# Kernel tuning notes

Measured on AMD Instinct MI355X. Metric: run time of the kernel, lower is better.

Reference implementation:

```python
import jax, jax.numpy as jnp
from jax import lax
import numpy as np

EPS_REG = 1.0     # ot.sinkhorn(..., M, 1, ...) hardcodes reg=1 in the original forward
N_ITER = 100      # max_iter: fixed stabilized (log-domain) Sinkhorn iterations


def setup_inputs() -> dict:
    key = jax.random.key(0)
    kx, ky = jax.random.split(key)
    x = jax.random.normal(kx, (1, 4096, 512), dtype=jnp.float32)
    y = jax.random.normal(ky, (1, 4096, 512), dtype=jnp.float32)
    return {"x": x, "y": y}


def _cost_matrix(x, y):
    x2 = jnp.sum(x * x, axis=-1)                      # [B, P1]
    y2 = jnp.sum(y * y, axis=-1)                      # [B, P2]
    xy = jnp.einsum("bpd,bqd->bpq", x, y)            # [B, P1, P2]
    return jnp.maximum(x2[:, :, None] + y2[:, None, :] - 2.0 * xy, 0.0)


def _sinkhorn_log(C, eps, n_iter):
    # Log-domain (stabilized) Sinkhorn with uniform marginals a=1/P1, b=1/P2.
    P1, P2 = C.shape
    eps_loga = eps * (-jnp.log(jnp.float32(P1)))
    eps_logb = eps * (-jnp.log(jnp.float32(P2)))

    def step(carry, _):
        f, g = carry
        f = eps_loga - eps * jax.nn.logsumexp((g[None, :] - C) / eps, axis=1)
        g = eps_logb - eps * jax.nn.logsumexp((f[:, None] - C) / eps, axis=0)
        return (f, g), None

    f0 = jnp.zeros((P1,), C.dtype)
    g0 = jnp.zeros((P2,), C.dtype)
    (f, g), _ = lax.scan(step, (f0, g0), None, length=n_iter)
    return jnp.exp((f[:, None] + g[None, :] - C) / eps)  # transport plan pi, rows sum to 1/P1


def reference(x, y):
    C = _cost_matrix(x, y)                                  # [B, P1, P2]
    pi = jax.vmap(lambda c: _sinkhorn_log(c, EPS_REG, N_ITER))(C)
    cost = jnp.sum(pi * C, axis=(-2, -1))                   # [B], reduction='none'
    return cost, pi, C
```

## Files before the change

kernel.cpp:

```cpp
#include <hip/hip_runtime.h>
#include <hip/hip_bf16.h>
#include <cstddef>

#define NROW 4096
#define DIM  512
static const size_t NP = (size_t)NROW * NROW;
#define ALPHA (-8.31776616671934f)

__global__ __launch_bounds__(256) void sqnorm_kernel(const float* __restrict__ x,
                                                     const float* __restrict__ y,
                                                     float* __restrict__ x2,
                                                     float* __restrict__ y2) {
    int gtid = blockIdx.x * 256 + threadIdx.x;
    int wid  = gtid >> 6;
    int lane = gtid & 63;
    const float* src = (wid < NROW) ? x : y;
    float*       dst = (wid < NROW) ? x2 : y2;
    int row = (wid < NROW) ? wid : (wid - NROW);
    const float4* r4 = (const float4*)(src + (size_t)row * DIM);
    float4 a = r4[lane];
    float4 b = r4[lane + 64];
    float s = a.x*a.x + a.y*a.y + a.z*a.z + a.w*a.w
            + b.x*b.x + b.y*b.y + b.z*b.z + b.w*b.w;
    #pragma unroll
    for (int off = 32; off > 0; off >>= 1) s += __shfl_down(s, off);
    if (lane == 0) dst[row] = s;
}

__global__ __launch_bounds__(256) void gemm_kernel(const float* __restrict__ A,
                                                   const float* __restrict__ B,
                                                   float* __restrict__ S) {
    __shared__ float As[16][132];
    __shared__ float Bs[16][132];
    const int bm = blockIdx.y * 128, bn = blockIdx.x * 128;
    const int tid = threadIdx.x;
    const int tx = tid & 15, ty = tid >> 4;
    float acc[8][8];
    #pragma unroll
    for (int i = 0; i < 8; ++i)
        #pragma unroll
        for (int j = 0; j < 8; ++j) acc[i][j] = 0.f;

    for (int kt = 0; kt < DIM; kt += 16) {
        #pragma unroll
        for (int h = 0; h < 2; ++h) {
            int f = tid + h * 256;
            int row = f >> 2, kk = (f & 3) << 2;
            float4 a4 = *(const float4*)(A + (size_t)(bm + row) * DIM + kt + kk);
            As[kk+0][row] = a4.x; As[kk+1][row] = a4.y;
            As[kk+2][row] = a4.z; As[kk+3][row] = a4.w;
            float4 b4 = *(const float4*)(B + (size_t)(bn + row) * DIM + kt + kk);
            Bs[kk+0][row] = b4.x; Bs[kk+1][row] = b4.y;
            Bs[kk+2][row] = b4.z; Bs[kk+3][row] = b4.w;
        }
        __syncthreads();
        #pragma unroll
        for (int k = 0; k < 16; ++k) {
            float ar[8], br[8];
            #pragma unroll
            for (int i = 0; i < 8; ++i) ar[i] = As[k][ty*8 + i];
            #pragma unroll
            for (int j = 0; j < 8; ++j) br[j] = Bs[k][tx*8 + j];
            #pragma unroll
            for (int i = 0; i < 8; ++i)
                #pragma unroll
                for (int j = 0; j < 8; ++j)
                    acc[i][j] = __fmaf_rn(ar[i], br[j], acc[i][j]);
        }
        __syncthreads();
    }
    #pragma unroll
    for (int i = 0; i < 8; ++i) {
        size_t off = (size_t)(bm + ty*8 + i) * NROW + bn + tx*8;
        #pragma unroll
        for (int j = 0; j < 8; ++j) S[off + j] = 2.0f * acc[i][j];
    }
}

__global__ __launch_bounds__(256) void transpose_kernel(const float* __restrict__ in,
                                                        float* __restrict__ out) {
    __shared__ float tile[64][65];
    int bx = blockIdx.x * 64, by = blockIdx.y * 64;
    int tx = threadIdx.x & 63, tw = threadIdx.x >> 6;
    #pragma unroll
    for (int r = tw; r < 64; r += 4)
        tile[r][tx] = in[(size_t)(by + r) * NROW + bx + tx];
    __syncthreads();
    #pragma unroll
    for (int r = tw; r < 64; r += 4)
        out[(size_t)(bx + r) * NROW + by + tx] = tile[tx][r];
}

__global__ void init_kernel(const float* __restrict__ y2,
                            float* __restrict__ gt,
                            float* __restrict__ cost) {
    int i = blockIdx.x * 256 + threadIdx.x;
    if (i < NROW) gt[i] = -y2[i];
    if (i == 0) cost[0] = 0.f;
}

__global__ __launch_bounds__(256) void lse_pass_kernel(const float* __restrict__ M,
                                                       const float* __restrict__ u,
                                                       float* __restrict__ outv) {
    const int row = blockIdx.x;
    const float* mrow = M + (size_t)row * NROW;
    const int t = threadIdx.x;
    float m = -3.0e38f, s = 0.f;
    #pragma unroll
    for (int h = 0; h < 16; ++h) {
        int j = t + h * 256;
        float v = u[j] + mrow[j];
        float d = v - m;
        float e = __expf(-fabsf(d));
        s = (d > 0.f) ? __fmaf_rn(s, e, 1.0f) : (s + e);
        m = fmaxf(m, v);
    }
    #pragma unroll
    for (int off = 1; off < 64; off <<= 1) {
        float m2 = __shfl_xor(m, off);
        float s2 = __shfl_xor(s, off);
        float d = m - m2;
        float e = __expf(-fabsf(d));
        s = (d > 0.f) ? __fmaf_rn(s2, e, s) : __fmaf_rn(s, e, s2);
        m = fmaxf(m, m2);
    }
    __shared__ float sm[4], ss[4];
    int lane = t & 63, w = t >> 6;
    if (lane == 0) { sm[w] = m; ss[w] = s; }
    __syncthreads();
    if (t == 0) {
        float M0 = sm[0], S0 = ss[0];
        #pragma unroll
        for (int w2 = 1; w2 < 4; ++w2) {
            float m2 = sm[w2], s2 = ss[w2];
            float d = M0 - m2;
            float e = __expf(-fabsf(d));
            S0 = (d > 0.f) ? __fmaf_rn(s2, e, S0) : __fmaf_rn(S0, e, s2);
            M0 = fmaxf(M0, m2);
        }
        outv[row] = ALPHA - (M0 + __logf(S0));
    }
}

__global__ __launch_bounds__(256) void finalize_kernel(const float* __restrict__ S,
                                                       const float* __restrict__ ft,
                                                       const float* __restrict__ gt,
                                                       const float* __restrict__ x2,
                                                       const float* __restrict__ y2,
                                                       float* __restrict__ pi,
                                                       float* __restrict__ C,
                                                       float* __restrict__ cost) {
    const int row = blockIdx.x;
    const size_t base = (size_t)row * NROW;
    const float fi  = ft[row];
    const float x2i = x2[row];
    float acc = 0.f;
    #pragma unroll
    for (int h = 0; h < 16; ++h) {
        int j = threadIdx.x + h * 256;
        float sv = S[base + j];
        float p  = __expf(fi + gt[j] + sv);
        float c  = fmaxf(x2i + y2[j] - sv, 0.f);
        pi[base + j] = p;
        C[base + j]  = c;
        acc = __fmaf_rn(p, c, acc);
    }
    #pragma unroll
    for (int off = 32; off > 0; off >>= 1) acc += __shfl_down(acc, off);
    __shared__ float sa[4];
    int lane = threadIdx.x & 63, w = threadIdx.x >> 6;
    if (lane == 0) sa[w] = acc;
    __syncthreads();
    if (threadIdx.x == 0)
        atomicAdd(cost, sa[0] + sa[1] + sa[2] + sa[3]);
}

extern "C" void kernel_launch(void* const* d_in, const int* in_sizes, int n_in,
                              void* d_out, int out_size, void* d_ws, size_t ws_size,
                              hipStream_t stream) {
    const float* x = (const float*)d_in[0];
    const float* y = (const float*)d_in[1];
    float* out  = (float*)d_out;
    float* cost = out;
    float* pi   = out + 1;
    float* Cpt  = out + 1 + NP;
    float* S  = Cpt;
    float* ST = pi;

    float* ws = (float*)d_ws;
    float* x2 = ws;
    float* y2 = ws + NROW;
    float* ft = ws + 2 * NROW;
    float* gt = ws + 3 * NROW;

    sqnorm_kernel<<<2048, 256, 0, stream>>>(x, y, x2, y2);
    gemm_kernel<<<dim3(32, 32), 256, 0, stream>>>(x, y, S);
    transpose_kernel<<<dim3(64, 64), 256, 0, stream>>>(S, ST);
    init_kernel<<<16, 256, 0, stream>>>(y2, gt, cost);

    for (int it = 0; it < 100; ++it) {
        lse_pass_kernel<<<NROW, 256, 0, stream>>>(S,  gt, ft);
        lse_pass_kernel<<<NROW, 256, 0, stream>>>(ST, ft, gt);
    }

    finalize_kernel<<<NROW, 256, 0, stream>>>(S, ft, gt, x2, y2, pi, Cpt, cost);
}
```

Measured before the change: 2.751 ms.

## Quantize cross-product matrix to int16 for Sinkhorn passes and use base-2 LSE

```diff
diff --git a/kernel.cpp b/kernel.cpp
--- a/kernel.cpp
+++ b/kernel.cpp
@@ -5,7 +5,12 @@
 #define NROW 4096
 #define DIM  512
 static const size_t NP = (size_t)NROW * NROW;
-#define ALPHA (-8.31776616671934f)
+#define L2E   1.4426950408889634f
+#define ALPHA2 (-12.0f)
+#define QSCALE 64.0f
+#define QD    (1.4426950408889634f / 64.0f)
+
+typedef unsigned int uint32;
 
 __global__ __launch_bounds__(256) void sqnorm_kernel(const float* __restrict__ x,
                                                      const float* __restrict__ y,
@@ -77,74 +82,120 @@
     }
 }
 
-__global__ __launch_bounds__(256) void transpose_kernel(const float* __restrict__ in,
-                                                        float* __restrict__ out) {
-    __shared__ float tile[64][65];
-    int bx = blockIdx.x * 64, by = blockIdx.y * 64;
-    int tx = threadIdx.x & 63, tw = threadIdx.x >> 6;
-    #pragma unroll
-    for (int r = tw; r < 64; r += 4)
-        tile[r][tx] = in[(size_t)(by + r) * NROW + bx + tx];
+__global__ __launch_bounds__(256) void quantA_kernel(const float* __restrict__ S,
+                                                     uint32* __restrict__ Sq) {
+    size_t i = (size_t)blockIdx.x * 256 + threadIdx.x;
+    const size_t nu = NP / 2, stride = (size_t)2048 * 256;
+    for (; i < nu; i += stride) {
+        float a = S[2*i], b = S[2*i + 1];
+        float qa = fmaxf(fminf(a * QSCALE,  32767.f), -32767.f);
+        float qb = fmaxf(fminf(b * QSCALE,  32767.f), -32767.f);
+        int ia = __float2int_rn(qa), ib = __float2int_rn(qb);
+        Sq[i] = (uint32)(ia & 0xffff) | ((uint32)ib << 16);
+    }
+}
+
+__global__ __launch_bounds__(256) void quantT_kernel(const float* __restrict__ S,
+                                                     uint32* __restrict__ SqT) {
+    __shared__ short tile[64][66];
+    const int bx = blockIdx.x * 64, by = blockIdx.y * 64;
+    const int t = threadIdx.x;
+    const int c = t & 63, r0 = t >> 6;
+    #pragma unroll
+    for (int rr = 0; rr < 16; ++rr) {
+        int r = r0 + rr * 4;
+        float v = S[(size_t)(by + r) * NROW + bx + c];
+        float q = fmaxf(fminf(v * QSCALE, 32767.f), -32767.f);
+        tile[r][c] = (short)__float2int_rn(q);
+    }
     __syncthreads();
-    #pragma unroll
-    for (int r = tw; r < 64; r += 4)
-        out[(size_t)(bx + r) * NROW + by + tx] = tile[tx][r];
+    const int p = t & 31, jl = t >> 5;
+    #pragma unroll
+    for (int jj = 0; jj < 8; ++jj) {
+        int j = jj * 8 + jl;
+        uint32 lo = (unsigned short)tile[2*p    ][j];
+        uint32 hi = (unsigned short)tile[2*p + 1][j];
+        SqT[(size_t)(bx + j) * (NROW/2) + (by >> 1) + p] = lo | (hi << 16);
+    }
 }
 
 __global__ void init_kernel(const float* __restrict__ y2,
-                            float* __restrict__ gt,
+                            float* __restrict__ gt2,
                             float* __restrict__ cost) {
     int i = blockIdx.x * 256 + threadIdx.x;
-    if (i < NROW) gt[i] = -y2[i];
+    if (i < NROW) gt2[i] = -y2[i] * L2E;
     if (i == 0) cost[0] = 0.f;
 }
 
-__global__ __launch_bounds__(256) void lse_pass_kernel(const float* __restrict__ M,
-                                                       const float* __restrict__ u,
-                                                       float* __restrict__ outv) {
-    const int row = blockIdx.x;
-    const float* mrow = M + (size_t)row * NROW;
+__global__ __launch_bounds__(256) void lseq_kernel(const uint32* __restrict__ Q,
+                                                   const float* __restrict__ u2,
+                                                   float* __restrict__ o2) {
+    const int r0 = blockIdx.x * 2;
+    const uint32* q0 = Q + (size_t)r0 * (NROW/2);
+    const uint32* q1 = q0 + (NROW/2);
     const int t = threadIdx.x;
-    float m = -3.0e38f, s = 0.f;
-    #pragma unroll
-    for (int h = 0; h < 16; ++h) {
-        int j = t + h * 256;
-        float v = u[j] + mrow[j];
-        float d = v - m;
-        float e = __expf(-fabsf(d));
-        s = (d > 0.f) ? __fmaf_rn(s, e, 1.0f) : (s + e);
-        m = fmaxf(m, v);
+    float m0 = -1e30f, s0 = 0.f, m1 = -1e30f, s1 = 0.f;
+    #pragma unroll
+    for (int h = 0; h < 8; ++h) {
+        int k = t + h * 256;
+        float2 uu = *(const float2*)(u2 + 2*k);
+        uint32 w0 = q0[k], w1 = q1[k];
+        float a0 = (float)(int)(short)(w0 & 0xffffu);
+        float b0 = (float)((int)w0 >> 16);
+        float a1 = (float)(int)(short)(w1 & 0xffffu);
+        float b1 = (float)((int)w1 >> 16);
+        float v00 = fmaf(a0, QD, uu.x), v01 = fmaf(b0, QD, uu.y);
+        float v10 = fmaf(a1, QD, uu.x), v11 = fmaf(b1, QD, uu.y);
+        float vm0 = fmaxf(v00, v01), vm1 = fmaxf(v10, v11);
+        if (__any(vm0 > m0 + 60.f)) {
+            float mn = fmaxf(m0, vm0);
+            s0 *= exp2f(m0 - mn); m0 = mn;
+        }
+        if (__any(vm1 > m1 + 60.f)) {
+            float mn = fmaxf(m1, vm1);
+            s1 *= exp2f(m1 - mn); m1 = mn;
+        }
+        s0 += exp2f(v00 - m0) + exp2f(v01 - m0);
+        s1 += exp2f(v10 - m1) + exp2f(v11 - m1);
     }
     #pragma unroll
     for (int off = 1; off < 64; off <<= 1) {
-        float m2 = __shfl_xor(m, off);
-        float s2 = __shfl_xor(s, off);
-        float d = m - m2;
-        float e = __expf(-fabsf(d));
-        s = (d > 0.f) ? __fmaf_rn(s2, e, s) : __fmaf_rn(s, e, s2);
-        m = fmaxf(m, m2);
-    }
-    __shared__ float sm[4], ss[4];
+        float mo = __shfl_xor(m0, off), so = __shfl_xor(s0, off);
+        float d = m0 - mo;
+        float e = exp2f(-fabsf(d));
+        s0 = (d > 0.f) ? fmaf(so, e, s0) : fmaf(s0, e, so);
+        m0 = fmaxf(m0, mo);
+        float mo1 = __shfl_xor(m1, off), so1 = __shfl_xor(s1, off);
+        float d1 = m1 - mo1;
+        float e1 = exp2f(-fabsf(d1));
+        s1 = (d1 > 0.f) ? fmaf(so1, e1, s1) : fmaf(s1, e1, so1);
+        m1 = fmaxf(m1, mo1);
+    }
+    __shared__ float sm0[4], ss0[4], sm1[4], ss1[4];
     int lane = t & 63, w = t >> 6;
-    if (lane == 0) { sm[w] = m; ss[w] = s; }
+    if (lane == 0) { sm0[w] = m0; ss0[w] = s0; sm1[w] = m1; ss1[w] = s1; }
     __syncthreads();
     if (t == 0) {
-        float M0 = sm[0], S0 = ss[0];
-        #pragma unroll
-        for (int w2 = 1; w2 < 4; ++w2) {
-            float m2 = sm[w2], s2 = ss[w2];
-            float d = M0 - m2;
-            float e = __expf(-fabsf(d));
-            S0 = (d > 0.f) ? __fmaf_rn(s2, e, S0) : __fmaf_rn(S0, e, s2);
-            M0 = fmaxf(M0, m2);
-        }
-        outv[row] = ALPHA - (M0 + __logf(S0));
+        float M0 = sm0[0], S0 = ss0[0], M1 = sm1[0], S1 = ss1[0];
+        #pragma unroll
+        for (int ww = 1; ww < 4; ++ww) {
+            float d = M0 - sm0[ww];
+            float e = exp2f(-fabsf(d));
+            S0 = (d > 0.f) ? fmaf(ss0[ww], e, S0) : fmaf(S0, e, ss0[ww]);
+            M0 = fmaxf(M0, sm0[ww]);
+            float d1 = M1 - sm1[ww];
+            float e1 = exp2f(-fabsf(d1));
+            S1 = (d1 > 0.f) ? fmaf(ss1[ww], e1, S1) : fmaf(S1, e1, ss1[ww]);
+            M1 = fmaxf(M1, sm1[ww]);
+        }
+        o2[r0]     = ALPHA2 - (M0 + __log2f(S0));
+        o2[r0 + 1] = ALPHA2 - (M1 + __log2f(S1));
     }
 }
 
 __global__ __launch_bounds__(256) void finalize_kernel(const float* __restrict__ S,
-                                                       const float* __restrict__ ft,
-                                                       const float* __restrict__ gt,
+                                                       const float* __restrict__ ft2,
+                                                       const float* __restrict__ gt2,
                                                        const float* __restrict__ x2,
                                                        const float* __restrict__ y2,
                                                        float* __restrict__ pi,
@@ -152,14 +203,14 @@
                                                        float* __restrict__ cost) {
     const int row = blockIdx.x;
     const size_t base = (size_t)row * NROW;
-    const float fi  = ft[row];
+    const float fi2 = ft2[row];
     const float x2i = x2[row];
     float acc = 0.f;
     #pragma unroll
     for (int h = 0; h < 16; ++h) {
         int j = threadIdx.x + h * 256;
         float sv = S[base + j];
-        float p  = __expf(fi + gt[j] + sv);
+        float p  = exp2f(fmaf(sv, L2E, fi2 + gt2[j]));
         float c  = fmaxf(x2i + y2[j] - sv, 0.f);
         pi[base + j] = p;
         C[base + j]  = c;
@@ -184,24 +235,26 @@
     float* cost = out;
     float* pi   = out + 1;
     float* Cpt  = out + 1 + NP;
-    float* S  = Cpt;
-    float* ST = pi;
-
-    float* ws = (float*)d_ws;
-    float* x2 = ws;
-    float* y2 = ws + NROW;
-    float* ft = ws + 2 * NROW;
-    float* gt = ws + 3 * NROW;
+    float* S    = Cpt;
+    uint32* Sq  = (uint32*)pi;
+    uint32* SqT = Sq + NP/2;
+
+    float* ws  = (float*)d_ws;
+    float* x2  = ws;
+    float* y2  = ws + NROW;
+    float* ft2 = ws + 2 * NROW;
+    float* gt2 = ws + 3 * NROW;
 
     sqnorm_kernel<<<2048, 256, 0, stream>>>(x, y, x2, y2);
     gemm_kernel<<<dim3(32, 32), 256, 0, stream>>>(x, y, S);
-    transpose_kernel<<<dim3(64, 64), 256, 0, stream>>>(S, ST);
-    init_kernel<<<16, 256, 0, stream>>>(y2, gt, cost);
+    quantA_kernel<<<2048, 256, 0, stream>>>(S, Sq);
+    quantT_kernel<<<dim3(64, 64), 256, 0, stream>>>(S, SqT);
+    init_kernel<<<16, 256, 0, stream>>>(y2, gt2, cost);
 
     for (int it = 0; it < 100; ++it) {
-        lse_pass_kernel<<<NROW, 256, 0, stream>>>(S,  gt, ft);
-        lse_pass_kernel<<<NROW, 256, 0, stream>>>(ST, ft, gt);
-    }
-
-    finalize_kernel<<<NROW, 256, 0, stream>>>(S, ft, gt, x2, y2, pi, Cpt, cost);
-}
+        lseq_kernel<<<2048, 256, 0, stream>>>(Sq,  gt2, ft2);
+        lseq_kernel<<<2048, 256, 0, stream>>>(SqT, ft2, gt2);
+    }
+
+    finalize_kernel<<<NROW, 256, 0, stream>>>(S, ft2, gt2, x2, y2, pi, Cpt, cost);
+}
```

New measurement: 2.921 ms. 1.06x slower.
